# Kernel optimization log

Measured on AMD Instinct MI355X. Metric: run time of the kernel, lower is better.

Reference implementation:

```python
import jax, jax.numpy as jnp
import numpy as np

B, N, M, IN, OUT, H = 256, 2048, 64, 128, 64, 100
EPS = 1e-8


def setup_inputs() -> dict:
    key = jax.random.key(0)
    ks = jax.random.split(key, 32)
    rn = lambda i, shp, sc=1.0: jax.random.normal(ks[i], shp, jnp.float32) * sc
    d = {}
    d["x"] = rn(0, (B, IN))
    d["Wc"] = rn(1, (IN, H), 1.0 / np.sqrt(IN)); d["bc"] = jnp.zeros((H,), jnp.float32)
    d["Wo"] = rn(2, (M, OUT), 1.0 / np.sqrt(M)); d["bo"] = jnp.zeros((OUT,), jnp.float32)
    i = 3
    for p in ("r", "w"):
        d[p + "_W_beta"] = rn(i, (H, 1), 0.1); i += 1; d[p + "_b_beta"] = jnp.zeros((1,), jnp.float32)
        d[p + "_W_gamma"] = rn(i, (H, 1), 0.1); i += 1; d[p + "_b_gamma"] = jnp.zeros((1,), jnp.float32)
        d[p + "_W_g"] = rn(i, (H, 1), 0.1); i += 1; d[p + "_b_g"] = jnp.zeros((1,), jnp.float32)
        # tiny shift weights + positive bias keep the shifted weighting positive
        # (the original code takes tilde_w ** gamma, which NaNs for negative base)
        d[p + "_W_s"] = rn(i, (H, 3), 0.001); i += 1; d[p + "_b_s"] = jnp.full((3,), 0.5, jnp.float32)
        d[p + "_W_k"] = rn(i, (H, M), 0.1); i += 1; d[p + "_b_k"] = jnp.zeros((M,), jnp.float32)
    d["w_W_e"] = rn(i, (H, M), 0.1); i += 1; d["w_b_e"] = jnp.zeros((M,), jnp.float32)
    d["w_W_a"] = rn(i, (H, M), 0.1); i += 1; d["w_b_a"] = jnp.zeros((M,), jnp.float32)
    d["r_attn_bias"] = rn(i, (B, N)); i += 1
    d["w_attn_bias"] = rn(i, (B, N)); i += 1
    d["memory_bias"] = rn(i, (B, N, M))
    return d


def _addressing(mem, attn, k, beta, g, s, gamma):
    # cosine similarity of key k [B,M] against each memory row [B,N,M]
    kn = jnp.maximum(jnp.linalg.norm(k, axis=1, keepdims=True), EPS)        # [B,1]
    mn = jnp.maximum(jnp.linalg.norm(mem, axis=2), EPS)                     # [B,N]
    cos = jnp.einsum('bm,bnm->bn', k, mem) / (kn * mn)                      # [B,N]
    w_c = jax.nn.softmax(beta * cos, axis=-1)                               # beta [B,1]
    w_g = g * w_c + (1.0 - g) * attn                                        # interpolation
    # circular 3-tap convolution: tw[i] = s0*w[i-1] + s1*w[i] + s2*w[i+1]
    tw = (s[:, 0:1] * jnp.roll(w_g, 1, axis=1)
          + s[:, 1:2] * w_g
          + s[:, 2:3] * jnp.roll(w_g, -1, axis=1))
    p = tw ** gamma                                                         # sharpening
    return p / (EPS + p.sum(axis=1, keepdims=True))


def _forward(x, Wc, bc, Wo, bo,
             r_W_beta, r_b_beta, r_W_gamma, r_b_gamma, r_W_g, r_b_g,
             r_W_s, r_b_s, r_W_k, r_b_k,
             w_W_beta, w_b_beta, w_W_gamma, w_b_gamma, w_W_g, w_b_g,
             w_W_s, w_b_s, w_W_k, w_b_k,
             w_W_e, w_b_e, w_W_a, w_b_a,
             r_attn_bias, w_attn_bias, memory_bias):
    h = x @ Wc + bc                                                         # controller [B,100]

    # ---- send: write-head addressing + erase/add write ----
    beta_w = jax.nn.softplus(h @ w_W_beta + w_b_beta)
    gamma_w = 1.0 + jax.nn.softplus(h @ w_W_gamma + w_b_gamma)
    g_w = jax.nn.sigmoid(h @ w_W_g + w_b_g)
    s_w = h @ w_W_s + w_b_s
    k_w = h @ w_W_k + w_b_k
    w_attn0 = jax.nn.softmax(w_attn_bias, axis=1)
    w_attn = _addressing(memory_bias, w_attn0, k_w, beta_w, g_w, s_w, gamma_w)
    e = jax.nn.sigmoid(h @ w_W_e + w_b_e)                                   # [B,M]
    a = h @ w_W_a + w_b_a                                                   # [B,M]
    mem = (memory_bias * (1.0 - w_attn[:, :, None] * e[:, None, :])
           + w_attn[:, :, None] * a[:, None, :])                            # [B,N,M]

    # ---- receive: read-head addressing + read + output ----
    beta_r = jax.nn.softplus(h @ r_W_beta + r_b_beta)
    gamma_r = 1.0 + jax.nn.softplus(h @ r_W_gamma + r_b_gamma)
    g_r = jax.nn.sigmoid(h @ r_W_g + r_b_g)
    s_r = h @ r_W_s + r_b_s
    k_r = h @ r_W_k + r_b_k
    r_attn0 = jax.nn.softmax(r_attn_bias, axis=1)
    r_attn = _addressing(mem, r_attn0, k_r, beta_r, g_r, s_r, gamma_r)
    r = jnp.einsum('bn,bnm->bm', r_attn, mem)                               # read vector [B,M]
    out = jax.nn.sigmoid(r @ Wo + bo)                                       # [B,OUT]
    return out


def reference(x, Wc, bc, Wo, bo,
              r_W_beta, r_b_beta, r_W_gamma, r_b_gamma, r_W_g, r_b_g,
              r_W_s, r_b_s, r_W_k, r_b_k,
              w_W_beta, w_b_beta, w_W_gamma, w_b_gamma, w_W_g, w_b_g,
              w_W_s, w_b_s, w_W_k, w_b_k,
              w_W_e, w_b_e, w_W_a, w_b_a,
              r_attn_bias, w_attn_bias, memory_bias):
    return _forward(x, Wc, bc, Wo, bo,
                    r_W_beta, r_b_beta, r_W_gamma, r_b_gamma, r_W_g, r_b_g,
                    r_W_s, r_b_s, r_W_k, r_b_k,
                    w_W_beta, w_b_beta, w_W_gamma, w_b_gamma, w_W_g, w_b_g,
                    w_W_s, w_b_s, w_W_k, w_b_k,
                    w_W_e, w_b_e, w_W_a, w_b_a,
                    r_attn_bias, w_attn_bias, memory_bias)
```

## Files before the change

### kernel.cpp

```cpp
#include <hip/hip_runtime.h>
#include <hip/hip_bf16.h>
#include <math.h>

#define BB 256
#define NN 2048
#define MM 64
#define INF_ 128
#define HH 100
#define EPSF 1e-8f

struct Ptrs { const float* p[32]; };

__device__ __forceinline__ float softplusf(float x) {
    return fmaxf(x, 0.0f) + log1pf(__expf(-fabsf(x)));
}
__device__ __forceinline__ float sigmoidf(float x) {
    return 1.0f / (1.0f + __expf(-x));
}
__device__ __forceinline__ float fpowf(float x, float g) {
    return __expf(g * __logf(x));
}

__device__ __forceinline__ void bredN(float& a, float& b, bool ismax, float* red)
{
    #pragma unroll
    for (int m = 32; m; m >>= 1) {
        float ta = __shfl_xor(a, m), tb = __shfl_xor(b, m);
        if (ismax) { a = fmaxf(a, ta); b = fmaxf(b, tb); }
        else       { a += ta; b += tb; }
    }
    const int wid = threadIdx.x >> 6;
    if ((threadIdx.x & 63) == 0) { red[wid] = a; red[16 + wid] = b; }
    __syncthreads();
    float ra = red[0], rb = red[16];
    #pragma unroll
    for (int w = 1; w < 16; ++w) {
        if (ismax) { ra = fmaxf(ra, red[w]); rb = fmaxf(rb, red[16 + w]); }
        else       { ra += red[w]; rb += red[16 + w]; }
    }
    __syncthreads();
    a = ra; b = rb;
}

__global__ void __launch_bounds__(1024) k_fused(Ptrs in,
                                                const float* __restrict__ mb,
                                                float* __restrict__ out)
{
    __shared__ float xs[INF_];
    __shared__ float hs[HH];
    __shared__ float pk_w[MM], pk_r[MM], pe[MM], pa[MM];
    __shared__ float psc[20];
    __shared__ __align__(16) float summ_l[NN * 8];
    __shared__ float wcs[NN];
    __shared__ float ats[NN];
    __shared__ float watt[NN];
    __shared__ float ratt[NN];
    __shared__ float red[32];
    __shared__ float wp1[16 * 64];
    __shared__ float wp2[16 * 64];
    __shared__ float rv[64];

    const int b = blockIdx.x, tid = threadIdx.x;
    const int lane = tid & 63, wv = tid >> 6;
    const int grp = tid >> 3, l8 = tid & 7;

    if (tid < INF_) xs[tid] = in.p[0][b * INF_ + tid];
    __syncthreads();

    if (tid < HH) {
        const float* Wc = in.p[1];
        float acc = in.p[2][tid];
        #pragma unroll 8
        for (int i = 0; i < INF_; ++i)
            acc = fmaf(xs[i], Wc[i * HH + tid], acc);
        hs[tid] = acc;
    }
    __syncthreads();

    if (wv < 4) {
        const int m = lane;
        const float* W; const float* bi;
        if      (wv == 0) { W = in.p[23]; bi = in.p[24]; }
        else if (wv == 1) { W = in.p[13]; bi = in.p[14]; }
        else if (wv == 2) { W = in.p[25]; bi = in.p[26]; }
        else              { W = in.p[27]; bi = in.p[28]; }
        float acc = bi[m];
        #pragma unroll 10
        for (int j = 0; j < HH; ++j)
            acc = fmaf(hs[j], W[j * 64 + m], acc);
        if      (wv == 0) pk_w[m] = acc;
        else if (wv == 1) pk_r[m] = acc;
        else if (wv == 2) pe[m]   = sigmoidf(acc);
        else              pa[m]   = acc;
    } else {
        const int s = wv - 4;
        const float* W; float bia; int strd = 1, c = 0;
        if      (s == 0) { W = in.p[15]; bia = in.p[16][0]; }
        else if (s == 1) { W = in.p[17]; bia = in.p[18][0]; }
        else if (s == 2) { W = in.p[19]; bia = in.p[20][0]; }
        else if (s == 3) { W = in.p[5];  bia = in.p[6][0]; }
        else if (s == 4) { W = in.p[7];  bia = in.p[8][0]; }
        else if (s == 5) { W = in.p[9];  bia = in.p[10][0]; }
        else if (s < 9)  { W = in.p[21]; c = s - 6; bia = in.p[22][c]; strd = 3; }
        else             { W = in.p[11]; c = s - 9; bia = in.p[12][c]; strd = 3; }
        float v = 0.f;
        if (lane < HH)      v = hs[lane] * W[lane * strd + c];
        if (lane < HH - 64) v = fmaf(hs[lane + 64], W[(lane + 64) * strd + c], v);
        #pragma unroll
        for (int m2 = 32; m2; m2 >>= 1) v += __shfl_xor(v, m2);
        if (lane == 0) {
            float r = v + bia;
            if      (s == 0) psc[15] = softplusf(r);
            else if (s == 1) psc[2]  = 1.0f + softplusf(r);
            else if (s == 2) psc[4]  = sigmoidf(r);
            else if (s == 3) psc[16] = softplusf(r);
            else if (s == 4) psc[3]  = 1.0f + softplusf(r);
            else if (s == 5) psc[5]  = sigmoidf(r);
            else if (s < 9)  psc[6 + c] = r;
            else             psc[9 + c] = r;
        }
    }
    __syncthreads();

    if (wv == 0) {
        float v = pk_w[lane] * pk_w[lane];
        #pragma unroll
        for (int m2 = 32; m2; m2 >>= 1) v += __shfl_xor(v, m2);
        if (lane == 0) psc[0] = psc[15] / fmaxf(sqrtf(v), EPSF);
    }
    if (wv == 1) {
        float v = pk_r[lane] * pk_r[lane];
        #pragma unroll
        for (int m2 = 32; m2; m2 >>= 1) v += __shfl_xor(v, m2);
        if (lane == 0) psc[1] = psc[16] / fmaxf(sqrtf(v), EPSF);
    }
    if (wv == 2) {
        float v = pk_r[lane] * pa[lane];
        #pragma unroll
        for (int m2 = 32; m2; m2 >>= 1) v += __shfl_xor(v, m2);
        if (lane == 0) psc[12] = v;
    }
    if (wv == 3) {
        float v = pa[lane] * pa[lane];
        #pragma unroll
        for (int m2 = 32; m2; m2 >>= 1) v += __shfl_xor(v, m2);
        if (lane == 0) psc[13] = v;
    }
    __syncthreads();

    {
        float kw[8], kr[8], ev[8], av[8];
        #pragma unroll
        for (int j = 0; j < 8; ++j) {
            kw[j] = pk_w[l8 * 8 + j];
            kr[j] = pk_r[l8 * 8 + j];
            ev[j] = pe[l8 * 8 + j];
            av[j] = pa[l8 * 8 + j];
        }
        const float4* base = reinterpret_cast<const float4*>(mb + (size_t)b * NN * MM);

        #pragma unroll 4
        for (int it = 0; it < 16; ++it) {
            const int n = it * 128 + grp;
            float4 v0 = base[n * 16 + 2 * l8];
            float4 v1 = base[n * 16 + 2 * l8 + 1];
            float f[8] = {v0.x, v0.y, v0.z, v0.w, v1.x, v1.y, v1.z, v1.w};

            float acc[8];
            #pragma unroll
            for (int j = 0; j < 8; ++j) acc[j] = 0.f;
            #pragma unroll
            for (int j = 0; j < 8; ++j) {
                const float m = f[j], m2 = m * m;
                const float x = ev[j] * m, y = ev[j] * m2;
                acc[0] = fmaf(kw[j], m,  acc[0]);
                acc[1] = fmaf(kr[j], m,  acc[1]);
                acc[2] = fmaf(kr[j], x,  acc[2]);
                acc[3] += m2;
                acc[4] += y;
                acc[5] = fmaf(ev[j], y,  acc[5]);
                acc[6] = fmaf(av[j], m,  acc[6]);
                acc[7] = fmaf(av[j], x,  acc[7]);
            }

            float k1[4];
            #pragma unroll
            for (int k = 0; k < 4; ++k) {
                float snd = (l8 & 1) ? acc[2 * k] : acc[2 * k + 1];
                float rcv = __shfl_xor(snd, 1);
                k1[k] = ((l8 & 1) ? acc[2 * k + 1] : acc[2 * k]) + rcv;
            }
            float k2[2];
            #pragma unroll
            for (int k = 0; k < 2; ++k) {
                float snd = (l8 & 2) ? k1[2 * k] : k1[2 * k + 1];
                float rcv = __shfl_xor(snd, 2);
                k2[k] = ((l8 & 2) ? k1[2 * k + 1] : k1[2 * k]) + rcv;
            }
            float snd = (l8 & 4) ? k2[0] : k2[1];
            float rcv = __shfl_xor(snd, 4);
            summ_l[n * 8 + l8] = ((l8 & 4) ? k2[1] : k2[0]) + rcv;
        }
    }
    __syncthreads();

    const float kra = psc[12], saa = psc[13];

    {
        const float g = psc[4], gamma = psc[2];
        const float s0c = psc[6], s1c = psc[7], s2c = psc[8];
        const float coef = psc[0];

        float mL = -1e30f, mB = -1e30f;
        #pragma unroll
        for (int k = 0; k < 2; ++k) {
            int i = tid + k * 1024;
            const float4 q0 = reinterpret_cast<const float4*>(summ_l + i * 8)[0];
            float lg = coef * q0.x / fmaxf(sqrtf(q0.w), EPSF);
            wcs[i] = lg; mL = fmaxf(mL, lg);
            float bb = in.p[30][(size_t)b * NN + i]; ats[i] = bb; mB = fmaxf(mB, bb);
        }
        __syncthreads();
        bredN(mL, mB, true, red);

        float sL = 0.f, sB = 0.f;
        #pragma unroll
        for (int k = 0; k < 2; ++k) {
            int i = tid + k * 1024;
            float ew = __expf(wcs[i] - mL);
            float eb = __expf(ats[i] - mB);
            wcs[i] = ew; ats[i] = eb;
            sL += ew; sB += eb;
        }
        bredN(sL, sB, false, red);
        const float iL = 1.0f / sL, iB = 1.0f / sB;

        #pragma unroll
        for (int k = 0; k < 2; ++k) {
            int i = tid + k * 1024;
            ats[i] = g * wcs[i] * iL + (1.0f - g) * ats[i] * iB;
        }
        __syncthreads();

        float pv[2]; float ps = 0.f;
        #pragma unroll
        for (int k = 0; k < 2; ++k) {
            int i = tid + k * 1024;
            float tw = s0c * ats[(i + NN - 1) & (NN - 1)]
                     + s1c * ats[i]
                     + s2c * ats[(i + 1) & (NN - 1)];
            float p = fpowf(tw, gamma);
            pv[k] = p; ps += p;
        }
        float dmy = 0.f;
        bredN(ps, dmy, false, red);
        const float inv = 1.0f / (EPSF + ps);
        #pragma unroll
        for (int k = 0; k < 2; ++k) {
            int i = tid + k * 1024;
            watt[i] = pv[k] * inv;
        }
        __syncthreads();
    }

    {
        const float g = psc[5], gamma = psc[3];
        const float s0c = psc[9], s1c = psc[10], s2c = psc[11];
        const float coef = psc[1];

        float mL = -1e30f, mB = -1e30f;
        #pragma unroll
        for (int k = 0; k < 2; ++k) {
            int i = tid + k * 1024;
            const float4* sp = reinterpret_cast<const float4*>(summ_l + i * 8);
            const float4 q0 = sp[0];
            const float4 q1 = sp[1];
            const float w = watt[i];
            const float dot = q0.y + w * (kra - q0.z);
            float nrm2 = q0.w + 2.f * w * (q1.z - q1.x)
                       + w * w * (q1.y + saa - 2.f * q1.w);
            nrm2 = fmaxf(nrm2, 0.f);
            float lg = coef * dot / fmaxf(sqrtf(nrm2), EPSF);
            wcs[i] = lg; mL = fmaxf(mL, lg);
            float bb = in.p[29][(size_t)b * NN + i]; ats[i] = bb; mB = fmaxf(mB, bb);
        }
        __syncthreads();
        bredN(mL, mB, true, red);

        float sL = 0.f, sB = 0.f;
        #pragma unroll
        for (int k = 0; k < 2; ++k) {
            int i = tid + k * 1024;
            float ew = __expf(wcs[i] - mL);
            float eb = __expf(ats[i] - mB);
            wcs[i] = ew; ats[i] = eb;
            sL += ew; sB += eb;
        }
        bredN(sL, sB, false, red);
        const float iL = 1.0f / sL, iB = 1.0f / sB;

        #pragma unroll
        for (int k = 0; k < 2; ++k) {
            int i = tid + k * 1024;
            ats[i] = g * wcs[i] * iL + (1.0f - g) * ats[i] * iB;
        }
        __syncthreads();

        float pv[2]; float ps = 0.f;
        #pragma unroll
        for (int k = 0; k < 2; ++k) {
            int i = tid + k * 1024;
            float tw = s0c * ats[(i + NN - 1) & (NN - 1)]
                     + s1c * ats[i]
                     + s2c * ats[(i + 1) & (NN - 1)];
            float p = fpowf(tw, gamma);
            pv[k] = p; ps += p;
        }
        float dmy = 0.f;
        bredN(ps, dmy, false, red);
        const float inv = 1.0f / (EPSF + ps);
        #pragma unroll
        for (int k = 0; k < 2; ++k) {
            int i = tid + k * 1024;
            ratt[i] = pv[k] * inv;
        }
        __syncthreads();
    }

    float tval = ratt[tid] * watt[tid] + ratt[tid + 1024] * watt[tid + 1024];
    {
        float dmy = 0.f;
        bredN(tval, dmy, false, red);
    }

    {
        float a1[8], a2[8];
        #pragma unroll
        for (int j = 0; j < 8; ++j) { a1[j] = 0.f; a2[j] = 0.f; }
        const float4* base = reinterpret_cast<const float4*>(mb + (size_t)b * NN * MM);

        #pragma unroll 4
        for (int it = 0; it < 16; ++it) {
            const int n = it * 128 + grp;
            const float c1 = ratt[n];
            const float c2 = c1 * watt[n];
            float4 v0 = base[n * 16 + 2 * l8];
            float4 v1 = base[n * 16 + 2 * l8 + 1];
            float f[8] = {v0.x, v0.y, v0.z, v0.w, v1.x, v1.y, v1.z, v1.w};
            #pragma unroll
            for (int j = 0; j < 8; ++j) {
                a1[j] = fmaf(c1, f[j], a1[j]);
                a2[j] = fmaf(c2, f[j], a2[j]);
            }
        }
        #pragma unroll
        for (int j = 0; j < 8; ++j) {
            #pragma unroll
            for (int mask = 8; mask < 64; mask <<= 1) {
                a1[j] += __shfl_xor(a1[j], mask);
                a2[j] += __shfl_xor(a2[j], mask);
            }
        }
        if (lane < 8) {
            #pragma unroll
            for (int j = 0; j < 8; ++j) {
                wp1[wv * 64 + lane * 8 + j] = a1[j];
                wp2[wv * 64 + lane * 8 + j] = a2[j];
            }
        }
    }
    __syncthreads();

    if (tid < 64) {
        float S1 = 0.f, S2 = 0.f;
        #pragma unroll
        for (int w8 = 0; w8 < 16; ++w8) {
            S1 += wp1[w8 * 64 + tid];
            S2 += wp2[w8 * 64 + tid];
        }
        rv[tid] = S1 - pe[tid] * S2 + tval * pa[tid];
    }
    __syncthreads();

    if (tid < 64) {
        const float* Wo = in.p[3];
        float o = in.p[4][tid];
        #pragma unroll 4
        for (int m = 0; m < 64; ++m) o = fmaf(rv[m], Wo[m * 64 + tid], o);
        out[(size_t)b * 64 + tid] = sigmoidf(o);
    }
}

extern "C" void kernel_launch(void* const* d_in, const int* in_sizes, int n_in,
                              void* d_out, int out_size, void* d_ws, size_t ws_size,
                              hipStream_t stream)
{
    Ptrs in;
    for (int i = 0; i < 32; ++i) in.p[i] = (const float*)d_in[i];
    const float* mb = (const float*)d_in[31];

    k_fused<<<BB, 1024, 0, stream>>>(in, mb, (float*)d_out);
}
```

Before: 62.97 us.

## Shrink shared memory by folding per-row sums into six padded arrays

The per-row memory statistics are reformulated algebraically from eight sums into six precombined quantities. These are stored in a padded struct-of-arrays layout instead of an 8-wide interleaved buffer. The wcs buffer is dropped in favour of registers, and the wp1/wp2 scratch now aliases the statistics buffer. Together with a launch-bounds occupancy hint, this cuts LDS use per block and removes a barrier per addressing pass, aiming at higher occupancy and fewer shared-memory accesses, at the cost of some reordering of floating-point arithmetic.

```diff
diff --git a/kernel.cpp b/kernel.cpp
--- a/kernel.cpp
+++ b/kernel.cpp
@@ -8,6 +8,7 @@
 #define INF_ 128
 #define HH 100
 #define EPSF 1e-8f
+#define PITCH (NN + 1)
 
 struct Ptrs { const float* p[32]; };
 
@@ -42,22 +43,19 @@
     a = ra; b = rb;
 }
 
-__global__ void __launch_bounds__(1024) k_fused(Ptrs in,
-                                                const float* __restrict__ mb,
-                                                float* __restrict__ out)
+__global__ void __launch_bounds__(1024, 8) k_fused(Ptrs in,
+                                                   const float* __restrict__ mb,
+                                                   float* __restrict__ out)
 {
     __shared__ float xs[INF_];
     __shared__ float hs[HH];
     __shared__ float pk_w[MM], pk_r[MM], pe[MM], pa[MM];
     __shared__ float psc[20];
-    __shared__ __align__(16) float summ_l[NN * 8];
-    __shared__ float wcs[NN];
+    __shared__ float summ6[6 * PITCH];
     __shared__ float ats[NN];
     __shared__ float watt[NN];
     __shared__ float ratt[NN];
     __shared__ float red[32];
-    __shared__ float wp1[16 * 64];
-    __shared__ float wp2[16 * 64];
     __shared__ float rv[64];
 
     const int b = blockIdx.x, tid = threadIdx.x;
@@ -157,6 +155,7 @@
             ev[j] = pe[l8 * 8 + j];
             av[j] = pa[l8 * 8 + j];
         }
+        const float kra_ = psc[12], saa_ = psc[13];
         const float4* base = reinterpret_cast<const float4*>(mb + (size_t)b * NN * MM);
 
         #pragma unroll 4
@@ -171,16 +170,14 @@
             for (int j = 0; j < 8; ++j) acc[j] = 0.f;
             #pragma unroll
             for (int j = 0; j < 8; ++j) {
-                const float m = f[j], m2 = m * m;
-                const float x = ev[j] * m, y = ev[j] * m2;
-                acc[0] = fmaf(kw[j], m,  acc[0]);
-                acc[1] = fmaf(kr[j], m,  acc[1]);
-                acc[2] = fmaf(kr[j], x,  acc[2]);
-                acc[3] += m2;
-                acc[4] += y;
-                acc[5] = fmaf(ev[j], y,  acc[5]);
-                acc[6] = fmaf(av[j], m,  acc[6]);
-                acc[7] = fmaf(av[j], x,  acc[7]);
+                const float m = f[j];
+                const float em = ev[j] * m;
+                acc[0] = fmaf(kw[j], m, acc[0]);
+                acc[1] = fmaf(m, m, acc[1]);
+                acc[2] = fmaf(kr[j], m, acc[2]);
+                acc[3] = fmaf(kr[j], em, acc[3]);
+                acc[4] = fmaf(m, av[j] - em, acc[4]);
+                acc[5] = fmaf(em, fmaf(-2.f, av[j], em), acc[5]);
             }
 
             float k1[4];
@@ -199,38 +196,40 @@
             }
             float snd = (l8 & 4) ? k2[0] : k2[1];
             float rcv = __shfl_xor(snd, 4);
-            summ_l[n * 8 + l8] = ((l8 & 4) ? k2[1] : k2[0]) + rcv;
-        }
-    }
-    __syncthreads();
-
-    const float kra = psc[12], saa = psc[13];
+            float tot = ((l8 & 4) ? k2[1] : k2[0]) + rcv;
+
+            if (l8 == 3) tot = kra_ - tot;
+            if (l8 == 5) tot += saa_;
+            if (l8 < 6) summ6[l8 * PITCH + n] = tot;
+        }
+    }
+    __syncthreads();
 
     {
         const float g = psc[4], gamma = psc[2];
         const float s0c = psc[6], s1c = psc[7], s2c = psc[8];
         const float coef = psc[0];
 
+        float lgr[2], bbr[2];
         float mL = -1e30f, mB = -1e30f;
         #pragma unroll
         for (int k = 0; k < 2; ++k) {
             int i = tid + k * 1024;
-            const float4 q0 = reinterpret_cast<const float4*>(summ_l + i * 8)[0];
-            float lg = coef * q0.x / fmaxf(sqrtf(q0.w), EPSF);
-            wcs[i] = lg; mL = fmaxf(mL, lg);
-            float bb = in.p[30][(size_t)b * NN + i]; ats[i] = bb; mB = fmaxf(mB, bb);
-        }
-        __syncthreads();
+            float lw = summ6[i];
+            float s0 = summ6[PITCH + i];
+            float lg = coef * lw / fmaxf(sqrtf(s0), EPSF);
+            lgr[k] = lg; mL = fmaxf(mL, lg);
+            float bb = in.p[30][(size_t)b * NN + i]; bbr[k] = bb; mB = fmaxf(mB, bb);
+        }
         bredN(mL, mB, true, red);
 
+        float pw[2], pb[2];
         float sL = 0.f, sB = 0.f;
         #pragma unroll
         for (int k = 0; k < 2; ++k) {
-            int i = tid + k * 1024;
-            float ew = __expf(wcs[i] - mL);
-            float eb = __expf(ats[i] - mB);
-            wcs[i] = ew; ats[i] = eb;
-            sL += ew; sB += eb;
+            pw[k] = __expf(lgr[k] - mL);
+            pb[k] = __expf(bbr[k] - mB);
+            sL += pw[k]; sB += pb[k];
         }
         bredN(sL, sB, false, red);
         const float iL = 1.0f / sL, iB = 1.0f / sB;
@@ -238,7 +237,7 @@
         #pragma unroll
         for (int k = 0; k < 2; ++k) {
             int i = tid + k * 1024;
-            ats[i] = g * wcs[i] * iL + (1.0f - g) * ats[i] * iB;
+            ats[i] = g * pw[k] * iL + (1.0f - g) * pb[k] * iB;
         }
         __syncthreads();
 
@@ -268,33 +267,33 @@
         const float s0c = psc[9], s1c = psc[10], s2c = psc[11];
         const float coef = psc[1];
 
+        float lgr[2], bbr[2];
         float mL = -1e30f, mB = -1e30f;
         #pragma unroll
         for (int k = 0; k < 2; ++k) {
             int i = tid + k * 1024;
-            const float4* sp = reinterpret_cast<const float4*>(summ_l + i * 8);
-            const float4 q0 = sp[0];
-            const float4 q1 = sp[1];
-            const float w = watt[i];
-            const float dot = q0.y + w * (kra - q0.z);
-            float nrm2 = q0.w + 2.f * w * (q1.z - q1.x)
-                       + w * w * (q1.y + saa - 2.f * q1.w);
+            const float w  = watt[i];
+            const float s0 = summ6[PITCH + i];
+            const float d1 = summ6[2 * PITCH + i];
+            const float v1 = summ6[3 * PITCH + i];
+            const float u1 = summ6[4 * PITCH + i];
+            const float u2 = summ6[5 * PITCH + i];
+            const float dot = fmaf(w, v1, d1);
+            float nrm2 = s0 + 2.f * w * u1 + w * w * u2;
             nrm2 = fmaxf(nrm2, 0.f);
             float lg = coef * dot / fmaxf(sqrtf(nrm2), EPSF);
-            wcs[i] = lg; mL = fmaxf(mL, lg);
-            float bb = in.p[29][(size_t)b * NN + i]; ats[i] = bb; mB = fmaxf(mB, bb);
-        }
-        __syncthreads();
+            lgr[k] = lg; mL = fmaxf(mL, lg);
+            float bb = in.p[29][(size_t)b * NN + i]; bbr[k] = bb; mB = fmaxf(mB, bb);
+        }
         bredN(mL, mB, true, red);
 
+        float pw[2], pb[2];
         float sL = 0.f, sB = 0.f;
         #pragma unroll
         for (int k = 0; k < 2; ++k) {
-            int i = tid + k * 1024;
-            float ew = __expf(wcs[i] - mL);
-            float eb = __expf(ats[i] - mB);
-            wcs[i] = ew; ats[i] = eb;
-            sL += ew; sB += eb;
+            pw[k] = __expf(lgr[k] - mL);
+            pb[k] = __expf(bbr[k] - mB);
+            sL += pw[k]; sB += pb[k];
         }
         bredN(sL, sB, false, red);
         const float iL = 1.0f / sL, iB = 1.0f / sB;
@@ -302,7 +301,7 @@
         #pragma unroll
         for (int k = 0; k < 2; ++k) {
             int i = tid + k * 1024;
-            ats[i] = g * wcs[i] * iL + (1.0f - g) * ats[i] * iB;
+            ats[i] = g * pw[k] * iL + (1.0f - g) * pb[k] * iB;
         }
         __syncthreads();
 
@@ -326,6 +325,9 @@
         }
         __syncthreads();
     }
+
+    float* wp1 = summ6;
+    float* wp2 = summ6 + 1024;
 
     float tval = ratt[tid] * watt[tid] + ratt[tid + 1024] * watt[tid + 1024];
     {
```

New measurement: 65.19 us. 1.04x slower.
